# Kernel optimization log

Hardware: AMD Instinct MI355X
Metric: run time of the kernel (lower is better)

## Reference

```python
import jax, jax.numpy as jnp
import numpy as np

N, IN_C, HID, OUT_C = 50000, 128, 256, 40
L, G = 4, 2
GC = HID // G  # 128 channels per group
E = 600000
EPS = 1e-5


def _ln(h, g, b):
    mu = jnp.mean(h, axis=-1, keepdims=True)
    var = jnp.mean((h - mu) ** 2, axis=-1, keepdims=True)
    return (h - mu) * jax.lax.rsqrt(var + EPS) * g + b


def setup_inputs() -> dict:
    key = jax.random.key(0)
    ks = jax.random.split(key, 16)
    s = lambda k, shape, sc=0.05: jax.random.normal(k, shape, dtype=jnp.float32) * sc
    return {
        "x": jax.random.normal(ks[0], (N, IN_C), dtype=jnp.float32),
        "edge_index": jax.random.randint(ks[1], (2, E), 0, N, dtype=jnp.int64),
        "edge_weight": jax.random.uniform(ks[2], (E,), dtype=jnp.float32),
        "lin1_w": s(ks[3], (IN_C, HID)),
        "lin1_b": jnp.zeros((HID,), jnp.float32),
        "lin2_w": s(ks[4], (HID, OUT_C)),
        "lin2_b": jnp.zeros((OUT_C,), jnp.float32),
        "norm_g": jnp.ones((L, G, GC), jnp.float32),   # per-block LayerNorm gamma
        "norm_b": jnp.zeros((L, G, GC), jnp.float32),  # per-block LayerNorm beta
        "conv_w": s(ks[5], (L, G, GC, GC)),            # per-block GCNConv weight
        "conv_b": jnp.zeros((L, G, GC), jnp.float32),  # per-block GCNConv bias
        "fnorm_g": jnp.ones((HID,), jnp.float32),
        "fnorm_b": jnp.zeros((HID,), jnp.float32),
    }


def reference(x, edge_index, edge_weight, lin1_w, lin1_b, lin2_w, lin2_b,
              norm_g, norm_b, conv_w, conv_b, fnorm_g, fnorm_b):
    src, dst = edge_index[0], edge_index[1]
    h = x @ lin1_w + lin1_b  # [N, HID]
    for l in range(L):
        xs = jnp.split(h, G, axis=-1)  # G x [N, GC]
        ys = []
        y_in = xs[-1]  # GroupAddRev coupling: y_i = x_i + F_i(y_{i-1}), y_{-1} = x_{G-1}
        for g in range(G):
            # GNNBlock: LayerNorm -> ReLU -> GCNConv(normalize=False)
            z = jax.nn.relu(_ln(y_in, norm_g[l, g], norm_b[l, g]))
            z = z @ conv_w[l, g]                       # GCNConv linear
            msg = edge_weight[:, None] * z[src]        # [E, GC]
            agg = jax.ops.segment_sum(msg, dst, num_segments=N) + conv_b[l, g]
            y_in = xs[g] + agg
            ys.append(y_in)
        h = jnp.concatenate(ys, axis=-1)
    h = jax.nn.relu(_ln(h, fnorm_g, fnorm_b))
    return h @ lin2_w + lin2_b  # [N, OUT_C]
```

## Files before the change

kernel.cpp:

```cpp
#include <hip/hip_runtime.h>
#include <stdint.h>

#define NN    50000
#define INC   128
#define HIDC  256
#define OUTC  40
#define GCH   128
#define NL    4
#define NG    2
#define NEDGE 600000
#define EPSV  1e-5f

typedef __bf16 bf16x8 __attribute__((ext_vector_type(8)));
typedef float  f32x4  __attribute__((ext_vector_type(4)));
typedef unsigned short u16x4 __attribute__((ext_vector_type(4)));
typedef unsigned short u16x8 __attribute__((ext_vector_type(8)));

__device__ __forceinline__ float bf2f(unsigned short u) {
    union { float f; unsigned int i; } v;
    v.i = ((unsigned int)u) << 16;
    return v.f;
}
__device__ __forceinline__ unsigned short f2bf(float f) {
    union { float f; unsigned int i; } v;
    v.f = f;
    unsigned int u = v.i;
    u += 0x7FFFu + ((u >> 16) & 1u);
    return (unsigned short)(u >> 16);
}
__device__ __forceinline__ float ldf(const void* p, int is_f32, long long i) {
    if (is_f32) return ((const float*)p)[i];
    return bf2f(((const unsigned short*)p)[i]);
}
__device__ __forceinline__ bf16x8 ld8(const unsigned short* p) {
    return *(const bf16x8*)p;
}
__device__ __forceinline__ void gload_lds16(const void* g, void* l) {
    __builtin_amdgcn_global_load_lds(
        (const __attribute__((address_space(1))) unsigned int*)g,
        (__attribute__((address_space(3))) unsigned int*)l,
        16, 0, 0);
}

__global__ void k_marker(void* out, float val, int n) {
    int i = blockIdx.x * 256 + threadIdx.x;
    if (i < n) ((unsigned short*)out)[i] = f2bf(val);
}

__global__ void k_detect(const int* ei, const unsigned short* xprobe,
                         int* flags, int* deg) {
    int t = threadIdx.x;
    int gid = blockIdx.x * 256 + t;
    if (gid < NN) deg[gid] = 0;
    if (blockIdx.x == 0) {
        __shared__ int hi_or, wild_cnt;
        if (t == 0) { hi_or = 0; wild_cnt = 0; }
        __syncthreads();
        int acc = 0;
        for (int i = 0; i < 8; i++) acc |= ei[2 * (t + i * 256) + 1];
        if (acc) atomicOr(&hi_or, 1);
        int wild = 0;
        for (int i = 0; i < 2; i++) {
            unsigned short u = xprobe[t + i * 256];
            int e = (u >> 7) & 0xFF;
            if (e <= 0x30 || e >= 0xC0) wild++;
        }
        atomicAdd(&wild_cnt, wild);
        __syncthreads();
        if (t == 0) {
            flags[0] = hi_or ? 0 : 1;
            flags[1] = (wild_cnt > 32) ? 1 : 0;
        }
    }
}

#define CVT_W1  32768
#define CVT_CW  131072
#define CVT_W2  12288
#define CVT_TOT (CVT_W1 + CVT_CW + CVT_W2)

__global__ void k_convert(const void* w1, const void* cw, const void* w2,
                          const void* b1, const void* ng, const void* nb, const void* cb,
                          const void* fg, const void* fb, const void* b2,
                          const int* flags,
                          unsigned short* w1t, unsigned short* cwt, unsigned short* w2t,
                          float* b1f, float* ngf, float* nbf, float* cbf,
                          float* fgf, float* fbf, float* b2f) {
    int t = threadIdx.x;
    int f32 = flags[1];
    if (blockIdx.x == gridDim.x - 1) {
        b1f[t] = ldf(b1, f32, t);
        fgf[t] = ldf(fg, f32, t);
        fbf[t] = ldf(fb, f32, t);
        if (t < 48) b2f[t] = (t < OUTC) ? ldf(b2, f32, t) : 0.0f;
        for (int i = 0; i < 4; i++) {
            int j = t + i * 256;
            ngf[j] = ldf(ng, f32, j);
            nbf[j] = ldf(nb, f32, j);
            cbf[j] = ldf(cb, f32, j);
        }
        return;
    }
    long long j = (long long)blockIdx.x * 256 + t;
    if (j >= CVT_TOT) return;
    if (j < CVT_W1) {
        int n = (int)(j >> 7), k = (int)(j & 127);
        w1t[n * 128 + (k ^ ((n & 7) << 3))] = f2bf(ldf(w1, f32, (long long)k * HIDC + n));
    } else if (j < CVT_W1 + CVT_CW) {
        long long jj = j - CVT_W1;
        int lg = (int)(jj >> 14);
        int rem = (int)(jj & 16383);
        int n = rem >> 7, k = rem & 127;
        cwt[lg * 16384 + n * 128 + (k ^ ((n & 7) << 3))] =
            f2bf(ldf(cw, f32, (long long)lg * GCH * GCH + (long long)k * GCH + n));
    } else {
        long long jj = j - (CVT_W1 + CVT_CW);
        int n = (int)(jj >> 8), k = (int)(jj & 255);
        w2t[n * 256 + (k ^ ((n & 7) << 3))] =
            (n < OUTC) ? f2bf(ldf(w2, f32, (long long)k * OUTC + n)) : (unsigned short)0;
    }
}

__global__ void k_count(const int* __restrict__ ei, const int* __restrict__ flags,
                        int* __restrict__ deg) {
    int e = (blockIdx.x * 256 + threadIdx.x) * 2;
    if (e >= NEDGE) return;
    int d0, d1;
    if (flags[0]) {
        int4 v = *(const int4*)(ei + 2 * (NEDGE + e));
        d0 = v.x; d1 = v.z;
    } else {
        int2 v = *(const int2*)(ei + NEDGE + e);
        d0 = v.x; d1 = v.y;
    }
    atomicAdd(&deg[d0], 1);
    if (e + 1 < NEDGE) atomicAdd(&deg[d1], 1);
}

#define SCAN_B 49
__global__ void k_scan_a(const int* __restrict__ deg, int* __restrict__ bsum) {
    __shared__ int part[256];
    int b = blockIdx.x, t = threadIdx.x;
    int base = b * 1024 + t * 4;
    int s = 0;
#pragma unroll
    for (int j = 0; j < 4; j++) {
        int i = base + j;
        if (i < NN) s += deg[i];
    }
    part[t] = s;
    __syncthreads();
    for (int off = 128; off > 0; off >>= 1) {
        if (t < off) part[t] += part[t + off];
        __syncthreads();
    }
    if (t == 0) bsum[b] = part[0];
}

__global__ void k_scan_c(const int* __restrict__ deg, const int* __restrict__ bsum,
                         int* __restrict__ rowptr, int* __restrict__ cursor) {
    __shared__ int part[256];
    __shared__ int bbase;
    int b = blockIdx.x, t = threadIdx.x;
    if (t == 0) { int r = 0; for (int i = 0; i < b; i++) r += bsum[i]; bbase = r; }
    int base = b * 1024 + t * 4;
    int v[4];
    int s = 0;
#pragma unroll
    for (int j = 0; j < 4; j++) {
        int i = base + j;
        v[j] = (i < NN) ? deg[i] : 0;
        s += v[j];
    }
    part[t] = s;
    __syncthreads();
    for (int off = 1; off < 256; off <<= 1) {
        int x = (t >= off) ? part[t - off] : 0;
        __syncthreads();
        part[t] += x;
        __syncthreads();
    }
    int run = bbase + part[t] - s;
#pragma unroll
    for (int j = 0; j < 4; j++) {
        int i = base + j;
        if (i < NN) { rowptr[i] = run; cursor[i] = run; }
        run += v[j];
    }
    if (b == SCAN_B - 1 && t == 255) rowptr[NN] = NEDGE;
}

__global__ void k_fill(const int* __restrict__ ei, const void* __restrict__ ew,
                       const int* __restrict__ flags,
                       int* __restrict__ cursor, unsigned int* __restrict__ epk) {
    int e = (blockIdx.x * 256 + threadIdx.x) * 2;
    if (e >= NEDGE) return;
    int is64 = flags[0];
    int f32 = flags[1];
    int d0, s0, d1 = 0, s1 = 0;
    int has1 = (e + 1 < NEDGE);
    if (is64) {
        d0 = ei[2 * (NEDGE + e)];
        s0 = ei[2 * e];
        if (has1) { d1 = ei[2 * (NEDGE + e) + 2]; s1 = ei[2 * e + 2]; }
    } else {
        d0 = ei[NEDGE + e];
        s0 = ei[e];
        if (has1) { d1 = ei[NEDGE + e + 1]; s1 = ei[e + 1]; }
    }
    int p0 = atomicAdd(&cursor[d0], 1);
    int p1 = has1 ? atomicAdd(&cursor[d1], 1) : 0;
    unsigned int w0 = f2bf(ldf(ew, f32, e));
    epk[p0] = (w0 << 16) | (unsigned int)s0;
    if (has1) {
        unsigned int w1 = f2bf(ldf(ew, f32, e + 1));
        epk[p1] = (w1 << 16) | (unsigned int)s1;
    }
}

__global__ __launch_bounds__(256, 5) void k_first(
    const void* __restrict__ x,
    const unsigned short* __restrict__ w1t,
    const float* __restrict__ b1f,
    const float* __restrict__ ngf, const float* __restrict__ nbf,
    const unsigned short* __restrict__ cw0,
    const int* __restrict__ flags,
    unsigned short* __restrict__ h,
    unsigned short* __restrict__ z0)
{
    __shared__ __align__(16) unsigned short xb[64 * 128];
    __shared__ __align__(16) unsigned short wt[64 * 128];
    int t = threadIdx.x;
    int r0 = blockIdx.x * 64;
    int f32x = flags[1];
    int w = t >> 6, lane = t & 63, quad = lane >> 4, ln = lane & 15;
    const f32x4 zf = {0.f, 0.f, 0.f, 0.f};

#pragma unroll
    for (int i = 0; i < 4; i++) {
        int cb = (i * 256 + t) * 16;
        gload_lds16((const char*)w1t + cb, (char*)wt + cb);
    }
#pragma unroll
    for (int i = 0; i < 4; i++) {
        int chunk = i * 256 + t;
        int row = chunk >> 4, c16 = chunk & 15;
        int grow = r0 + row;
        u16x8 val = {0, 0, 0, 0, 0, 0, 0, 0};
        if (grow < NN) {
            if (f32x) {
                const float* p = (const float*)x + (long long)grow * INC + c16 * 8;
                float4 a = *(const float4*)p;
                float4 c = *(const float4*)(p + 4);
                val[0] = f2bf(a.x); val[1] = f2bf(a.y); val[2] = f2bf(a.z); val[3] = f2bf(a.w);
                val[4] = f2bf(c.x); val[5] = f2bf(c.y); val[6] = f2bf(c.z); val[7] = f2bf(c.w);
            } else {
                val = *(const u16x8*)((const unsigned short*)x + (long long)grow * INC + c16 * 8);
            }
        }
        *(u16x8*)((char*)xb + row * 256 + ((c16 * 16) ^ ((row & 7) << 4))) = val;
    }
    __syncthreads();

    f32x4 acc[2][8];
#pragma unroll
    for (int i = 0; i < 2; i++)
#pragma unroll
        for (int j = 0; j < 8; j++) acc[i][j] = zf;

#pragma unroll
    for (int ph = 0; ph < 4; ph++) {
        int nh = ph >> 1, s = ph & 1;
#pragma unroll
        for (int kk = 0; kk < 4; kk++) {
            int cb = kk * 64 + quad * 16;
            int rA = w * 16 + ln;
            bf16x8 a = *(const bf16x8*)((const char*)xb + rA * 256 + (cb ^ ((rA & 7) << 4)));
#pragma unroll
            for (int nfl = 0; nfl < 4; nfl++) {
                int rB = nfl * 16 + ln;
                bf16x8 b = *(const bf16x8*)((const char*)wt + rB * 256 + (cb ^ ((rB & 7) << 4)));
                acc[nh][s * 4 + nfl] =
                    __builtin_amdgcn_mfma_f32_16x16x32_bf16(a, b, acc[nh][s * 4 + nfl], 0, 0, 0);
            }
        }
        __syncthreads();
        if (ph < 3) {
#pragma unroll
            for (int i = 0; i < 4; i++) {
                int cb = (i * 256 + t) * 16;
                gload_lds16((const char*)w1t + (ph + 1) * 16384 + cb, (char*)wt + cb);
            }
            __syncthreads();
        }
    }

#pragma unroll
    for (int i = 0; i < 4; i++) {
        int cb = (i * 256 + t) * 16;
        gload_lds16((const char*)cw0 + cb, (char*)wt + cb);
    }

    float ga8[8], be8[8], yv[8][4];
#pragma unroll
    for (int nf = 0; nf < 8; nf++) {
        int col = nf * 16 + ln;
        float b0 = b1f[col], b1 = b1f[128 + col];
        ga8[nf] = ngf[col]; be8[nf] = nbf[col];
#pragma unroll
        for (int r4 = 0; r4 < 4; r4++) {
            int row = r0 + w * 16 + quad * 4 + r4;
            unsigned short h0 = f2bf(acc[0][nf][r4] + b0);
            unsigned short h1 = f2bf(acc[1][nf][r4] + b1);
            if (row < NN) {
                h[(long long)row * HIDC + col] = h0;
                h[(long long)row * HIDC + 128 + col] = h1;
            }
            yv[nf][r4] = bf2f(h1);
        }
    }
    unsigned short* a_tile = xb;
#pragma unroll
    for (int r4 = 0; r4 < 4; r4++) {
        float s = 0.f, q = 0.f;
#pragma unroll
        for (int nf = 0; nf < 8; nf++) { s += yv[nf][r4]; q += yv[nf][r4] * yv[nf][r4]; }
        s += __shfl_xor(s, 1, 64); s += __shfl_xor(s, 2, 64);
        s += __shfl_xor(s, 4, 64); s += __shfl_xor(s, 8, 64);
        q += __shfl_xor(q, 1, 64); q += __shfl_xor(q, 2, 64);
        q += __shfl_xor(q, 4, 64); q += __shfl_xor(q, 8, 64);
        float mu = s * (1.0f / GCH);
        float var = q * (1.0f / GCH) - mu * mu;
        float rs = rsqrtf(var + EPSV);
        int row = w * 16 + quad * 4 + r4;
#pragma unroll
        for (int nf = 0; nf < 8; nf++) {
            float val = (yv[nf][r4] - mu) * rs * ga8[nf] + be8[nf];
            if (val < 0.f) val = 0.f;
            *(unsigned short*)((char*)a_tile + row * 256 +
                               (((nf * 16 + ln) * 2) ^ ((row & 7) << 4))) = f2bf(val);
        }
    }
    __syncthreads();

    f32x4 acc2[8];
#pragma unroll
    for (int j = 0; j < 8; j++) acc2[j] = zf;
#pragma unroll
    for (int s = 0; s < 2; s++) {
#pragma unroll
        for (int kk = 0; kk < 4; kk++) {
            int cb = kk * 64 + quad * 16;
            int rA = w * 16 + ln;
            bf16x8 a = *(const bf16x8*)((const char*)a_tile + rA * 256 + (cb ^ ((rA & 7) << 4)));
#pragma unroll
            for (int nfl = 0; nfl < 4; nfl++) {
                int rB = nfl * 16 + ln;
                bf16x8 b = *(const bf16x8*)((const char*)wt + rB * 256 + (cb ^ ((rB & 7) << 4)));
                acc2[s * 4 + nfl] =
                    __builtin_amdgcn_mfma_f32_16x16x32_bf16(a, b, acc2[s * 4 + nfl], 0, 0, 0);
            }
        }
        if (s == 0) {
            __syncthreads();
#pragma unroll
            for (int i = 0; i < 4; i++) {
                int cb = (i * 256 + t) * 16;
                gload_lds16((const char*)cw0 + 16384 + cb, (char*)wt + cb);
            }
            __syncthreads();
        }
    }
#pragma unroll
    for (int nf = 0; nf < 8; nf++) {
        int col = nf * 16 + ln;
#pragma unroll
        for (int r4 = 0; r4 < 4; r4++) {
            int row2 = r0 + w * 16 + quad * 4 + r4;
            if (row2 < NN) z0[(long long)row2 * GCH + col] = f2bf(acc2[nf][r4]);
        }
    }
}

__global__ __launch_bounds__(256, 5) void k_fused(
    const int* __restrict__ rowptr, const unsigned int* __restrict__ epk,
    const unsigned short* __restrict__ zin,
    const float* __restrict__ cb,
    unsigned short* __restrict__ h, int out_half,
    const float* __restrict__ ga, const float* __restrict__ be,
    const unsigned short* __restrict__ cwn,
    unsigned short* __restrict__ zout)
{
    __shared__ __align__(16) unsigned short wt[64 * 128];
    __shared__ __align__(16) unsigned short a_tile[64 * 128];
    int t = threadIdx.x;
    int r0 = blockIdx.x * 64;
    int c8 = (t & 15) << 3;

#pragma unroll
    for (int i = 0; i < 4; i++) {
        int cbyte = (i * 256 + t) * 16;
        gload_lds16((const char*)cwn + cbyte, (char*)wt + cbyte);
    }

#pragma unroll 1
    for (int bt = 0; bt < 4; bt++) {
        int row = bt * 16 + (t >> 4);
        int node = r0 + row;
        if (node < NN) {
            int beg = rowptr[node], end = rowptr[node + 1];
            unsigned short* hp = h + (long long)node * HIDC + out_half * GCH + c8;
            u16x8 hv = *(u16x8*)hp;
            const unsigned short* zb = zin + c8;
            float acc[8];
#pragma unroll
            for (int j = 0; j < 8; j++) acc[j] = 0.f;

            int e = beg;
            for (; e + 7 < end; e += 8) {
                unsigned int pe[8];
                u16x8 v[8];
#pragma unroll
                for (int i = 0; i < 8; i++) pe[i] = epk[e + i];
#pragma unroll
                for (int i = 0; i < 8; i++)
                    v[i] = *(const u16x8*)(zb + (long long)(pe[i] & 0xFFFFu) * GCH);
#pragma unroll
                for (int i = 0; i < 8; i++) {
                    float wv = bf2f((unsigned short)(pe[i] >> 16));
#pragma unroll
                    for (int j = 0; j < 8; j++) acc[j] += wv * bf2f(v[i][j]);
                }
            }
            if (e + 3 < end) {
                unsigned int pe[4];
                u16x8 v[4];
#pragma unroll
                for (int i = 0; i < 4; i++) pe[i] = epk[e + i];
#pragma unroll
                for (int i = 0; i < 4; i++)
                    v[i] = *(const u16x8*)(zb + (long long)(pe[i] & 0xFFFFu) * GCH);
#pragma unroll
                for (int i = 0; i < 4; i++) {
                    float wv = bf2f((unsigned short)(pe[i] >> 16));
#pragma unroll
                    for (int j = 0; j < 8; j++) acc[j] += wv * bf2f(v[i][j]);
                }
                e += 4;
            }
            for (; e < end; e++) {
                unsigned int pe = epk[e];
                float w0 = bf2f((unsigned short)(pe >> 16));
                u16x8 v = *(const u16x8*)(zb + (long long)(pe & 0xFFFFu) * GCH);
#pragma unroll
                for (int j = 0; j < 8; j++) acc[j] += w0 * bf2f(v[j]);
            }

            float y[8]; float sum = 0.f, sq = 0.f;
#pragma unroll
            for (int j = 0; j < 8; j++) {
                float yy = bf2f(hv[j]) + acc[j] + cb[c8 + j];
                unsigned short r = f2bf(yy);
                hv[j] = r;
                y[j] = bf2f(r);
                sum += y[j]; sq += y[j] * y[j];
            }
            *(u16x8*)hp = hv;

            sum += __shfl_xor(sum, 1, 64); sum += __shfl_xor(sum, 2, 64);
            sum += __shfl_xor(sum, 4, 64); sum += __shfl_xor(sum, 8, 64);
            sq  += __shfl_xor(sq, 1, 64);  sq  += __shfl_xor(sq, 2, 64);
            sq  += __shfl_xor(sq, 4, 64);  sq  += __shfl_xor(sq, 8, 64);
            float mu = sum * (1.0f / GCH);
            float var = sq * (1.0f / GCH) - mu * mu;
            float rs = rsqrtf(var + EPSV);
            u16x8 o;
#pragma unroll
            for (int j = 0; j < 8; j++) {
                float val = (y[j] - mu) * rs * ga[c8 + j] + be[c8 + j];
                if (val < 0.f) val = 0.f;
                o[j] = f2bf(val);
            }
            *(u16x8*)((char*)a_tile + row * 256 + ((c8 * 2) ^ ((row & 7) << 4))) = o;
        }
    }
    __syncthreads();

    int w = t >> 6, lane = t & 63, quad = lane >> 4, ln = lane & 15;
    const f32x4 zf = {0.f, 0.f, 0.f, 0.f};
    f32x4 acc2[8];
#pragma unroll
    for (int j = 0; j < 8; j++) acc2[j] = zf;
#pragma unroll
    for (int s = 0; s < 2; s++) {
#pragma unroll
        for (int kk = 0; kk < 4; kk++) {
            int cbyte = kk * 64 + quad * 16;
            int rA = w * 16 + ln;
            bf16x8 a = *(const bf16x8*)((const char*)a_tile + rA * 256 + (cbyte ^ ((rA & 7) << 4)));
#pragma unroll
            for (int nfl = 0; nfl < 4; nfl++) {
                int rB = nfl * 16 + ln;
                bf16x8 b = *(const bf16x8*)((const char*)wt + rB * 256 + (cbyte ^ ((rB & 7) << 4)));
                acc2[s * 4 + nfl] =
                    __builtin_amdgcn_mfma_f32_16x16x32_bf16(a, b, acc2[s * 4 + nfl], 0, 0, 0);
            }
        }
        if (s == 0) {
            __syncthreads();
#pragma unroll
            for (int i = 0; i < 4; i++) {
                int cbyte = (i * 256 + t) * 16;
                gload_lds16((const char*)cwn + 16384 + cbyte, (char*)wt + cbyte);
            }
            __syncthreads();
        }
    }
#pragma unroll
    for (int nf = 0; nf < 8; nf++) {
        int col = nf * 16 + ln;
#pragma unroll
        for (int r4 = 0; r4 < 4; r4++) {
            int row2 = r0 + w * 16 + quad * 4 + r4;
            if (row2 < NN) zout[(long long)row2 * GCH + col] = f2bf(acc2[nf][r4]);
        }
    }
}

__global__ __launch_bounds__(256, 5) void k_last(
    const int* __restrict__ rowptr, const unsigned int* __restrict__ epk,
    const unsigned short* __restrict__ zin,
    const float* __restrict__ cb,
    unsigned short* __restrict__ h,
    const float* __restrict__ fgf, const float* __restrict__ fbf,
    const unsigned short* __restrict__ w2t,
    const float* __restrict__ b2f,
    const int* __restrict__ flags,
    void* __restrict__ out)
{
    __shared__ __align__(16) unsigned short a_tile[64 * 256];
    int t = threadIdx.x;
    int r0 = blockIdx.x * 64;
    int c8 = (t & 15) << 3;
    const int out_half = 1;

#pragma unroll 1
    for (int bt = 0; bt < 4; bt++) {
        int row = bt * 16 + (t >> 4);
        int node = r0 + row;
        if (node < NN) {
            int beg = rowptr[node], end = rowptr[node + 1];
            unsigned short* hp = h + (long long)node * HIDC + out_half * GCH + c8;
            u16x8 hv = *(u16x8*)hp;
            const unsigned short* zb = zin + c8;
            float acc[8];
#pragma unroll
            for (int j = 0; j < 8; j++) acc[j] = 0.f;

            int e = beg;
            for (; e + 7 < end; e += 8) {
                unsigned int pe[8];
                u16x8 v[8];
#pragma unroll
                for (int i = 0; i < 8; i++) pe[i] = epk[e + i];
#pragma unroll
                for (int i = 0; i < 8; i++)
                    v[i] = *(const u16x8*)(zb + (long long)(pe[i] & 0xFFFFu) * GCH);
#pragma unroll
                for (int i = 0; i < 8; i++) {
                    float wv = bf2f((unsigned short)(pe[i] >> 16));
#pragma unroll
                    for (int j = 0; j < 8; j++) acc[j] += wv * bf2f(v[i][j]);
                }
            }
            if (e + 3 < end) {
                unsigned int pe[4];
                u16x8 v[4];
#pragma unroll
                for (int i = 0; i < 4; i++) pe[i] = epk[e + i];
#pragma unroll
                for (int i = 0; i < 4; i++)
                    v[i] = *(const u16x8*)(zb + (long long)(pe[i] & 0xFFFFu) * GCH);
#pragma unroll
                for (int i = 0; i < 4; i++) {
                    float wv = bf2f((unsigned short)(pe[i] >> 16));
#pragma unroll
                    for (int j = 0; j < 8; j++) acc[j] += wv * bf2f(v[i][j]);
                }
                e += 4;
            }
            for (; e < end; e++) {
                unsigned int pe = epk[e];
                float w0 = bf2f((unsigned short)(pe >> 16));
                u16x8 v = *(const u16x8*)(zb + (long long)(pe & 0xFFFFu) * GCH);
#pragma unroll
                for (int j = 0; j < 8; j++) acc[j] += w0 * bf2f(v[j]);
            }

            float y[8]; float sum = 0.f, sq = 0.f;
#pragma unroll
            for (int j = 0; j < 8; j++) {
                float yy = bf2f(hv[j]) + acc[j] + cb[c8 + j];
                unsigned short r = f2bf(yy);
                hv[j] = r;
                y[j] = bf2f(r);
                sum += y[j]; sq += y[j] * y[j];
            }
            *(u16x8*)hp = hv;

            float oy[8];
            u16x8 ov = *(const u16x8*)(h + (long long)node * HIDC + (out_half ^ 1) * GCH + c8);
#pragma unroll
            for (int j = 0; j < 8; j++) {
                oy[j] = bf2f(ov[j]);
                sum += oy[j]; sq += oy[j] * oy[j];
            }
            sum += __shfl_xor(sum, 1, 64); sum += __shfl_xor(sum, 2, 64);
            sum += __shfl_xor(sum, 4, 64); sum += __shfl_xor(sum, 8, 64);
            sq  += __shfl_xor(sq, 1, 64);  sq  += __shfl_xor(sq, 2, 64);
            sq  += __shfl_xor(sq, 4, 64);  sq  += __shfl_xor(sq, 8, 64);
            float mu = sum * (1.0f / HIDC);
            float var = sq * (1.0f / HIDC) - mu * mu;
            float rs = rsqrtf(var + EPSV);

            u16x8 o;
            int cn = out_half * GCH + c8;
#pragma unroll
            for (int j = 0; j < 8; j++) {
                float val = (y[j] - mu) * rs * fgf[cn + j] + fbf[cn + j];
                if (val < 0.f) val = 0.f;
                o[j] = f2bf(val);
            }
            *(u16x8*)((char*)a_tile + row * 512 + ((cn * 2) ^ ((row & 7) << 4))) = o;
            int co = (out_half ^ 1) * GCH + c8;
#pragma unroll
            for (int j = 0; j < 8; j++) {
                float val = (oy[j] - mu) * rs * fgf[co + j] + fbf[co + j];
                if (val < 0.f) val = 0.f;
                o[j] = f2bf(val);
            }
            *(u16x8*)((char*)a_tile + row * 512 + ((co * 2) ^ ((row & 7) << 4))) = o;
        }
    }
    __syncthreads();

    int w = t >> 6, lane = t & 63, quad = lane >> 4, ln = lane & 15;
    const f32x4 zf = {0.f, 0.f, 0.f, 0.f};
    f32x4 acc2[3];
#pragma unroll
    for (int j = 0; j < 3; j++) acc2[j] = zf;
#pragma unroll
    for (int kk = 0; kk < 8; kk++) {
        int cbyte = kk * 64 + quad * 16;
        int ko = kk * 32 + quad * 8;
        int row = w * 16 + ln;
        bf16x8 a = *(const bf16x8*)((const char*)a_tile + row * 512 + (cbyte ^ ((row & 7) << 4)));
#pragma unroll
        for (int nf = 0; nf < 3; nf++) {
            int rB = nf * 16 + ln;
            bf16x8 b = ld8(w2t + rB * 256 + (ko ^ ((rB & 7) << 3)));
            acc2[nf] = __builtin_amdgcn_mfma_f32_16x16x32_bf16(a, b, acc2[nf], 0, 0, 0);
        }
    }
    int f32o = flags[1];
#pragma unroll
    for (int nf = 0; nf < 3; nf++) {
        int col = nf * 16 + ln;
        if (col >= OUTC) continue;
        float bias = b2f[col];
#pragma unroll
        for (int r4 = 0; r4 < 4; r4++) {
            int row2 = r0 + w * 16 + quad * 4 + r4;
            if (row2 < NN) {
                float val = acc2[nf][r4] + bias;
                long long o = (long long)row2 * OUTC + col;
                if (f32o) ((float*)out)[o] = val;
                else      ((unsigned short*)out)[o] = f2bf(val);
            }
        }
    }
}

extern "C" void kernel_launch(void* const* d_in, const int* in_sizes, int n_in,
                              void* d_out, int out_size, void* d_ws, size_t ws_size,
                              hipStream_t stream)
{
    const void* x       = d_in[0];
    const int*  ei      = (const int*)d_in[1];
    const void* ew      = d_in[2];
    const void* lin1_w  = d_in[3];
    const void* lin1_b  = d_in[4];
    const void* lin2_w  = d_in[5];
    const void* lin2_b  = d_in[6];
    const void* norm_g  = d_in[7];
    const void* norm_b  = d_in[8];
    const void* conv_w  = d_in[9];
    const void* conv_b  = d_in[10];
    const void* fnorm_g = d_in[11];
    const void* fnorm_b = d_in[12];

    char* ws = (char*)d_ws;
    size_t off = 0;
    auto alloc = [&](size_t bytes) { void* p = (void*)(ws + off); off += (bytes + 255) & ~255ull; return p; };

    unsigned short* h      = (unsigned short*)alloc((size_t)NN * HIDC * 2);
    unsigned short* z0     = (unsigned short*)alloc((size_t)NN * GCH * 2);
    unsigned short* z1     = (unsigned short*)alloc((size_t)NN * GCH * 2);
    unsigned short* w1t    = (unsigned short*)alloc((size_t)CVT_W1 * 2);
    unsigned short* cwt    = (unsigned short*)alloc((size_t)CVT_CW * 2);
    unsigned short* w2t    = (unsigned short*)alloc((size_t)CVT_W2 * 2);
    float*          b1f    = (float*)alloc(256 * 4);
    float*          ngf    = (float*)alloc(1024 * 4);
    float*          nbf    = (float*)alloc(1024 * 4);
    float*          cbf    = (float*)alloc(1024 * 4);
    float*          fgf    = (float*)alloc(256 * 4);
    float*          fbf    = (float*)alloc(256 * 4);
    float*          b2f    = (float*)alloc(48 * 4);
    int*            deg    = (int*)alloc((size_t)NN * 4);
    int*            rowptr = (int*)alloc(((size_t)NN + 1) * 4);
    int*            cursor = (int*)alloc((size_t)NN * 4);
    unsigned int*   epk    = (unsigned int*)alloc((size_t)NEDGE * 4);
    int*            flags  = (int*)alloc(256);
    int*            bsum   = (int*)alloc(SCAN_B * 4);

    if (ws_size < off || n_in < 13) {
        float mv = 100.0f + (float)(ws_size >> 20) + ((n_in < 13) ? 10000.0f : 0.0f);
        k_marker<<<(out_size + 255) / 256, 256, 0, stream>>>(d_out, mv, out_size);
        return;
    }

    k_detect<<<196, 256, 0, stream>>>(ei, (const unsigned short*)x, flags, deg);
    k_convert<<<CVT_TOT / 256 + 1, 256, 0, stream>>>(lin1_w, conv_w, lin2_w,
                                                     lin1_b, norm_g, norm_b, conv_b,
                                                     fnorm_g, fnorm_b, lin2_b, flags,
                                                     w1t, cwt, w2t,
                                                     b1f, ngf, nbf, cbf, fgf, fbf, b2f);
    k_count<<<(NEDGE / 2 + 255) / 256, 256, 0, stream>>>(ei, flags, deg);
    k_scan_a<<<SCAN_B, 256, 0, stream>>>(deg, bsum);
    k_scan_c<<<SCAN_B, 256, 0, stream>>>(deg, bsum, rowptr, cursor);
    k_fill<<<(NEDGE / 2 + 255) / 256, 256, 0, stream>>>(ei, ew, flags, cursor, epk);

    const int GB = (NN + 63) / 64;
    k_first<<<GB, 256, 0, stream>>>(x, w1t, b1f, ngf, nbf, cwt, flags, h, z0);
    for (int lg = 0; lg < NL * NG - 1; lg++) {
        unsigned short* zin  = (lg & 1) ? z1 : z0;
        unsigned short* zout = (lg & 1) ? z0 : z1;
        k_fused<<<GB, 256, 0, stream>>>(rowptr, epk, zin, cbf + lg * GCH, h, lg & 1,
                                        ngf + (lg + 1) * GCH, nbf + (lg + 1) * GCH,
                                        cwt + (size_t)(lg + 1) * 16384, zout);
    }
    k_last<<<GB, 256, 0, stream>>>(rowptr, epk, z1, cbf + 7 * GCH, h,
                                   fgf, fbf, w2t, b2f, flags, d_out);
}
```

Measured before the change: 464.6 us.

## Merge preprocessing kernels to cut launches and hoist rowptr loads

The detect and convert kernels become one prep launch, in which the convert blocks recompute the dtype flag themselves. The two-pass scan becomes a single kernel where each block re-sums the preceding degrees. The edge-fill work moves into the first layer kernel as extra blocks. In the fused and last kernels, the rowptr loads for all four node batches are hoisted ahead of the loop. The aim is to remove launch gaps and serial dependencies in setup, at the cost of redundant prefix summation and duplicated flag detection.

```diff
diff --git a/kernel.cpp b/kernel.cpp
--- a/kernel.cpp
+++ b/kernel.cpp
@@ -47,48 +47,59 @@
     if (i < n) ((unsigned short*)out)[i] = f2bf(val);
 }
 
-__global__ void k_detect(const int* ei, const unsigned short* xprobe,
-                         int* flags, int* deg) {
-    int t = threadIdx.x;
-    int gid = blockIdx.x * 256 + t;
-    if (gid < NN) deg[gid] = 0;
-    if (blockIdx.x == 0) {
-        __shared__ int hi_or, wild_cnt;
-        if (t == 0) { hi_or = 0; wild_cnt = 0; }
-        __syncthreads();
-        int acc = 0;
-        for (int i = 0; i < 8; i++) acc |= ei[2 * (t + i * 256) + 1];
-        if (acc) atomicOr(&hi_or, 1);
-        int wild = 0;
-        for (int i = 0; i < 2; i++) {
-            unsigned short u = xprobe[t + i * 256];
-            int e = (u >> 7) & 0xFF;
-            if (e <= 0x30 || e >= 0xC0) wild++;
-        }
-        atomicAdd(&wild_cnt, wild);
-        __syncthreads();
-        if (t == 0) {
-            flags[0] = hi_or ? 0 : 1;
-            flags[1] = (wild_cnt > 32) ? 1 : 0;
-        }
-    }
-}
-
 #define CVT_W1  32768
 #define CVT_CW  131072
 #define CVT_W2  12288
 #define CVT_TOT (CVT_W1 + CVT_CW + CVT_W2)
 
-__global__ void k_convert(const void* w1, const void* cw, const void* w2,
-                          const void* b1, const void* ng, const void* nb, const void* cb,
-                          const void* fg, const void* fb, const void* b2,
-                          const int* flags,
-                          unsigned short* w1t, unsigned short* cwt, unsigned short* w2t,
-                          float* b1f, float* ngf, float* nbf, float* cbf,
-                          float* fgf, float* fbf, float* b2f) {
-    int t = threadIdx.x;
-    int f32 = flags[1];
-    if (blockIdx.x == gridDim.x - 1) {
+__global__ void k_prep(const void* x, const int* ei,
+                       const void* w1, const void* cw, const void* w2,
+                       const void* b1, const void* ng, const void* nb, const void* cb,
+                       const void* fg, const void* fb, const void* b2,
+                       int* flags, int* deg,
+                       unsigned short* w1t, unsigned short* cwt, unsigned short* w2t,
+                       float* b1f, float* ngf, float* nbf, float* cbf,
+                       float* fgf, float* fbf, float* b2f) {
+    int t = threadIdx.x, b = blockIdx.x;
+    if (b < 196) {
+        int gid = b * 256 + t;
+        if (gid < NN) deg[gid] = 0;
+        if (b == 0) {
+            __shared__ int hi_or, wild_cnt;
+            if (t == 0) { hi_or = 0; wild_cnt = 0; }
+            __syncthreads();
+            int acc = 0;
+            for (int i = 0; i < 8; i++) acc |= ei[2 * (t + i * 256) + 1];
+            if (acc) atomicOr(&hi_or, 1);
+            int wild = 0;
+            for (int i = 0; i < 2; i++) {
+                unsigned short u = ((const unsigned short*)x)[t + i * 256];
+                int e = (u >> 7) & 0xFF;
+                if (e <= 0x30 || e >= 0xC0) wild++;
+            }
+            atomicAdd(&wild_cnt, wild);
+            __syncthreads();
+            if (t == 0) {
+                flags[0] = hi_or ? 0 : 1;
+                flags[1] = (wild_cnt > 32) ? 1 : 0;
+            }
+        }
+        return;
+    }
+    __shared__ int wc;
+    if (t == 0) wc = 0;
+    __syncthreads();
+    int wild = 0;
+    for (int i = 0; i < 2; i++) {
+        unsigned short u = ((const unsigned short*)x)[t + i * 256];
+        int e = (u >> 7) & 0xFF;
+        if (e <= 0x30 || e >= 0xC0) wild++;
+    }
+    atomicAdd(&wc, wild);
+    __syncthreads();
+    int f32 = (wc > 32) ? 1 : 0;
+    int cb2 = b - 196;
+    if (cb2 == 688) {
         b1f[t] = ldf(b1, f32, t);
         fgf[t] = ldf(fg, f32, t);
         fbf[t] = ldf(fb, f32, t);
@@ -101,7 +112,7 @@
         }
         return;
     }
-    long long j = (long long)blockIdx.x * 256 + t;
+    long long j = (long long)cb2 * 256 + t;
     if (j >= CVT_TOT) return;
     if (j < CVT_W1) {
         int n = (int)(j >> 7), k = (int)(j & 127);
@@ -138,31 +149,23 @@
 }
 
 #define SCAN_B 49
-__global__ void k_scan_a(const int* __restrict__ deg, int* __restrict__ bsum) {
+__global__ void k_scan(const int* __restrict__ deg,
+                       int* __restrict__ rowptr, int* __restrict__ cursor) {
     __shared__ int part[256];
+    __shared__ int bbase_s;
     int b = blockIdx.x, t = threadIdx.x;
-    int base = b * 1024 + t * 4;
-    int s = 0;
-#pragma unroll
-    for (int j = 0; j < 4; j++) {
-        int i = base + j;
-        if (i < NN) s += deg[i];
-    }
-    part[t] = s;
+    int lim = b * 1024;
+    int pre = 0;
+    for (int i = t; i < lim; i += 256) pre += deg[i];
+    part[t] = pre;
     __syncthreads();
     for (int off = 128; off > 0; off >>= 1) {
         if (t < off) part[t] += part[t + off];
         __syncthreads();
     }
-    if (t == 0) bsum[b] = part[0];
-}
-
-__global__ void k_scan_c(const int* __restrict__ deg, const int* __restrict__ bsum,
-                         int* __restrict__ rowptr, int* __restrict__ cursor) {
-    __shared__ int part[256];
-    __shared__ int bbase;
-    int b = blockIdx.x, t = threadIdx.x;
-    if (t == 0) { int r = 0; for (int i = 0; i < b; i++) r += bsum[i]; bbase = r; }
+    if (t == 0) bbase_s = part[0];
+    __syncthreads();
+
     int base = b * 1024 + t * 4;
     int v[4];
     int s = 0;
@@ -180,7 +183,7 @@
         part[t] += x;
         __syncthreads();
     }
-    int run = bbase + part[t] - s;
+    int run = bbase_s + part[t] - s;
 #pragma unroll
     for (int j = 0; j < 4; j++) {
         int i = base + j;
@@ -190,35 +193,8 @@
     if (b == SCAN_B - 1 && t == 255) rowptr[NN] = NEDGE;
 }
 
-__global__ void k_fill(const int* __restrict__ ei, const void* __restrict__ ew,
-                       const int* __restrict__ flags,
-                       int* __restrict__ cursor, unsigned int* __restrict__ epk) {
-    int e = (blockIdx.x * 256 + threadIdx.x) * 2;
-    if (e >= NEDGE) return;
-    int is64 = flags[0];
-    int f32 = flags[1];
-    int d0, s0, d1 = 0, s1 = 0;
-    int has1 = (e + 1 < NEDGE);
-    if (is64) {
-        d0 = ei[2 * (NEDGE + e)];
-        s0 = ei[2 * e];
-        if (has1) { d1 = ei[2 * (NEDGE + e) + 2]; s1 = ei[2 * e + 2]; }
-    } else {
-        d0 = ei[NEDGE + e];
-        s0 = ei[e];
-        if (has1) { d1 = ei[NEDGE + e + 1]; s1 = ei[e + 1]; }
-    }
-    int p0 = atomicAdd(&cursor[d0], 1);
-    int p1 = has1 ? atomicAdd(&cursor[d1], 1) : 0;
-    unsigned int w0 = f2bf(ldf(ew, f32, e));
-    epk[p0] = (w0 << 16) | (unsigned int)s0;
-    if (has1) {
-        unsigned int w1 = f2bf(ldf(ew, f32, e + 1));
-        epk[p1] = (w1 << 16) | (unsigned int)s1;
-    }
-}
-
-__global__ __launch_bounds__(256, 5) void k_first(
+#define FIRST_B 782
+__global__ __launch_bounds__(256, 5) void k_firstfill(
     const void* __restrict__ x,
     const unsigned short* __restrict__ w1t,
     const float* __restrict__ b1f,
@@ -226,13 +202,42 @@
     const unsigned short* __restrict__ cw0,
     const int* __restrict__ flags,
     unsigned short* __restrict__ h,
-    unsigned short* __restrict__ z0)
+    unsigned short* __restrict__ z0,
+    const int* __restrict__ ei, const void* __restrict__ ew,
+    int* __restrict__ cursor, unsigned int* __restrict__ epk)
 {
     __shared__ __align__(16) unsigned short xb[64 * 128];
     __shared__ __align__(16) unsigned short wt[64 * 128];
     int t = threadIdx.x;
+    int f32x = flags[1];
+
+    if (blockIdx.x >= FIRST_B) {
+        int e = ((blockIdx.x - FIRST_B) * 256 + t) * 2;
+        if (e >= NEDGE) return;
+        int is64 = flags[0];
+        int d0, s0, d1 = 0, s1 = 0;
+        int has1 = (e + 1 < NEDGE);
+        if (is64) {
+            d0 = ei[2 * (NEDGE + e)];
+            s0 = ei[2 * e];
+            if (has1) { d1 = ei[2 * (NEDGE + e) + 2]; s1 = ei[2 * e + 2]; }
+        } else {
+            d0 = ei[NEDGE + e];
+            s0 = ei[e];
+            if (has1) { d1 = ei[NEDGE + e + 1]; s1 = ei[e + 1]; }
+        }
+        int p0 = atomicAdd(&cursor[d0], 1);
+        int p1 = has1 ? atomicAdd(&cursor[d1], 1) : 0;
+        unsigned int w0 = f2bf(ldf(ew, f32x, e));
+        epk[p0] = (w0 << 16) | (unsigned int)s0;
+        if (has1) {
+            unsigned int w1v = f2bf(ldf(ew, f32x, e + 1));
+            epk[p1] = (w1v << 16) | (unsigned int)s1;
+        }
+        return;
+    }
+
     int r0 = blockIdx.x * 64;
-    int f32x = flags[1];
     int w = t >> 6, lane = t & 63, quad = lane >> 4, ln = lane & 15;
     const f32x4 zf = {0.f, 0.f, 0.f, 0.f};
 
@@ -403,12 +408,20 @@
         gload_lds16((const char*)cwn + cbyte, (char*)wt + cbyte);
     }
 
+    int begA[4], endA[4];
+#pragma unroll
+    for (int bt = 0; bt < 4; bt++) {
+        int node = r0 + bt * 16 + (t >> 4);
+        begA[bt] = (node < NN) ? rowptr[node] : 0;
+        endA[bt] = (node < NN) ? rowptr[node + 1] : 0;
+    }
+
 #pragma unroll 1
     for (int bt = 0; bt < 4; bt++) {
         int row = bt * 16 + (t >> 4);
         int node = r0 + row;
         if (node < NN) {
-            int beg = rowptr[node], end = rowptr[node + 1];
+            int beg = begA[bt], end = endA[bt];
             unsigned short* hp = h + (long long)node * HIDC + out_half * GCH + c8;
             u16x8 hv = *(u16x8*)hp;
             const unsigned short* zb = zin + c8;
@@ -544,12 +557,20 @@
     int c8 = (t & 15) << 3;
     const int out_half = 1;
 
+    int begA[4], endA[4];
+#pragma unroll
+    for (int bt = 0; bt < 4; bt++) {
+        int node = r0 + bt * 16 + (t >> 4);
+        begA[bt] = (node < NN) ? rowptr[node] : 0;
+        endA[bt] = (node < NN) ? rowptr[node + 1] : 0;
+    }
+
 #pragma unroll 1
     for (int bt = 0; bt < 4; bt++) {
         int row = bt * 16 + (t >> 4);
         int node = r0 + row;
         if (node < NN) {
-            int beg = rowptr[node], end = rowptr[node + 1];
+            int beg = begA[bt], end = endA[bt];
             unsigned short* hp = h + (long long)node * HIDC + out_half * GCH + c8;
             u16x8 hv = *(u16x8*)hp;
             const unsigned short* zb = zin + c8;
@@ -721,7 +742,6 @@
     int*            cursor = (int*)alloc((size_t)NN * 4);
     unsigned int*   epk    = (unsigned int*)alloc((size_t)NEDGE * 4);
     int*            flags  = (int*)alloc(256);
-    int*            bsum   = (int*)alloc(SCAN_B * 4);
 
     if (ws_size < off || n_in < 13) {
         float mv = 100.0f + (float)(ws_size >> 20) + ((n_in < 13) ? 10000.0f : 0.0f);
@@ -729,26 +749,25 @@
         return;
     }
 
-    k_detect<<<196, 256, 0, stream>>>(ei, (const unsigned short*)x, flags, deg);
-    k_convert<<<CVT_TOT / 256 + 1, 256, 0, stream>>>(lin1_w, conv_w, lin2_w,
-                                                     lin1_b, norm_g, norm_b, conv_b,
-                                                     fnorm_g, fnorm_b, lin2_b, flags,
-                                                     w1t, cwt, w2t,
-                                                     b1f, ngf, nbf, cbf, fgf, fbf, b2f);
+    k_prep<<<885, 256, 0, stream>>>(x, ei, lin1_w, conv_w, lin2_w,
+                                    lin1_b, norm_g, norm_b, conv_b,
+                                    fnorm_g, fnorm_b, lin2_b,
+                                    flags, deg, w1t, cwt, w2t,
+                                    b1f, ngf, nbf, cbf, fgf, fbf, b2f);
     k_count<<<(NEDGE / 2 + 255) / 256, 256, 0, stream>>>(ei, flags, deg);
-    k_scan_a<<<SCAN_B, 256, 0, stream>>>(deg, bsum);
-    k_scan_c<<<SCAN_B, 256, 0, stream>>>(deg, bsum, rowptr, cursor);
-    k_fill<<<(NEDGE / 2 + 255) / 256, 256, 0, stream>>>(ei, ew, flags, cursor, epk);
-
-    const int GB = (NN + 63) / 64;
-    k_first<<<GB, 256, 0, stream>>>(x, w1t, b1f, ngf, nbf, cwt, flags, h, z0);
+    k_scan<<<SCAN_B, 256, 0, stream>>>(deg, rowptr, cursor);
+
+    const int FILL_B = (NEDGE / 2 + 255) / 256;
+    k_firstfill<<<FIRST_B + FILL_B, 256, 0, stream>>>(x, w1t, b1f, ngf, nbf, cwt,
+                                                      flags, h, z0,
+                                                      ei, ew, cursor, epk);
     for (int lg = 0; lg < NL * NG - 1; lg++) {
         unsigned short* zin  = (lg & 1) ? z1 : z0;
         unsigned short* zout = (lg & 1) ? z0 : z1;
-        k_fused<<<GB, 256, 0, stream>>>(rowptr, epk, zin, cbf + lg * GCH, h, lg & 1,
-                                        ngf + (lg + 1) * GCH, nbf + (lg + 1) * GCH,
-                                        cwt + (size_t)(lg + 1) * 16384, zout);
-    }
-    k_last<<<GB, 256, 0, stream>>>(rowptr, epk, z1, cbf + 7 * GCH, h,
-                                   fgf, fbf, w2t, b2f, flags, d_out);
-}
+        k_fused<<<FIRST_B, 256, 0, stream>>>(rowptr, epk, zin, cbf + lg * GCH, h, lg & 1,
+                                             ngf + (lg + 1) * GCH, nbf + (lg + 1) * GCH,
+                                             cwt + (size_t)(lg + 1) * 16384, zout);
+    }
+    k_last<<<FIRST_B, 256, 0, stream>>>(rowptr, epk, z1, cbf + 7 * GCH, h,
+                                        fgf, fbf, w2t, b2f, flags, d_out);
+}
```

Measured after the change: 497.4 us. 1.07x slower.
